# Performance work log

Measured on AMD Instinct MI355X. Metric: run time of the kernel, lower is better.

Reference implementation:

```python
import jax, jax.numpy as jnp
import numpy as np

DIM = 1024; DEPTH = 2; DSTATE = 128; HEADDIM = 64; DCONV = 4; EXPAND = 2
DINNER = EXPAND * DIM; NHEADS = DINNER // HEADDIM
CONVCH = DINNER + 2 * DSTATE          # x, B, C channels fed through depthwise conv
DINPROJ = 2 * DINNER + 2 * DSTATE + NHEADS  # z, xBC, dt
VOCAB = 256; EPS = 1e-5
B, T = 2, 1024


def _causal_conv(x, w, b):
    # depthwise causal conv1d: x [B,T,C], w [C,K], b [C]
    K = w.shape[1]
    xp = jnp.pad(x, ((0, 0), (K - 1, 0), (0, 0)))
    y = jnp.broadcast_to(b, x.shape)
    for k in range(K):
        y = y + xp[:, k:k + x.shape[1], :] * w[:, k]
    return y


def _mamba2_layer(h, Wp, cw, cb, dtb, alog, Dd, gw, Wo):
    Bb, Tt, _ = h.shape
    zxbcdt = jnp.einsum('btd,pd->btp', h, Wp)   # [B,T,DINPROJ]
    z = zxbcdt[..., :DINNER]
    xBC = zxbcdt[..., DINNER:DINNER + CONVCH]
    dt_raw = zxbcdt[..., DINNER + CONVCH:]
    xBC = jax.nn.silu(_causal_conv(xBC, cw, cb))
    xs = xBC[..., :DINNER].reshape(Bb, Tt, NHEADS, HEADDIM)
    Bm = xBC[..., DINNER:DINNER + DSTATE]        # [B,T,N] (ngroups=1)
    Cm = xBC[..., DINNER + DSTATE:]              # [B,T,N]
    dt = jax.nn.softplus(dt_raw + dtb)           # [B,T,H]
    dA = jnp.exp(dt * (-jnp.exp(alog)))          # [B,T,H]

    def step(s, inps):
        da_t, dt_t, x_t, b_t, c_t = inps
        dbx = dt_t[:, :, None, None] * x_t[..., None] * b_t[:, None, None, :]
        s = da_t[:, :, None, None] * s + dbx     # [B,H,P,N]
        y = jnp.einsum('bhpn,bn->bhp', s, c_t)
        return s, y

    s0 = jnp.zeros((Bb, NHEADS, HEADDIM, DSTATE), h.dtype)
    seq = (jnp.moveaxis(dA, 1, 0), jnp.moveaxis(dt, 1, 0), jnp.moveaxis(xs, 1, 0),
           jnp.moveaxis(Bm, 1, 0), jnp.moveaxis(Cm, 1, 0))
    _, ys = jax.lax.scan(step, s0, seq)          # ys [T,B,H,P]
    y = jnp.moveaxis(ys, 0, 1) + Dd[:, None] * xs
    y = y.reshape(Bb, Tt, DINNER) * jax.nn.silu(z)   # gated RMSNorm (norm(y*silu(z)))
    y = y * jax.lax.rsqrt(jnp.mean(y * y, -1, keepdims=True) + EPS) * gw
    return jnp.einsum('bti,di->btd', y, Wo)


def setup_inputs() -> dict:
    key = jax.random.key(0)
    ks = jax.random.split(key, 8)
    s = 0.02
    inp = {}
    inp['x'] = jax.random.randint(ks[0], (B, T), 0, VOCAB)
    inp['embed'] = jax.random.normal(ks[1], (VOCAB, DIM)) * s
    inp['in_proj_w'] = jax.random.normal(ks[2], (DEPTH, DINPROJ, DIM)) * s
    inp['conv_w'] = jax.random.normal(ks[3], (DEPTH, CONVCH, DCONV)) * 0.2
    inp['conv_b'] = jnp.zeros((DEPTH, CONVCH))
    # dt_bias so softplus(dt) ~ [1e-3, 1e-1]
    inp['dt_bias'] = jax.random.uniform(ks[4], (DEPTH, NHEADS), minval=-4.6, maxval=-2.0)
    inp['A_log'] = jnp.log(jnp.broadcast_to(jnp.arange(1, NHEADS + 1, dtype=jnp.float32), (DEPTH, NHEADS)))
    inp['D'] = jnp.ones((DEPTH, NHEADS))
    inp['gnorm_w'] = jnp.ones((DEPTH, DINNER))
    inp['out_proj_w'] = jax.random.normal(ks[5], (DEPTH, DIM, DINNER)) * s
    inp['final_norm_w'] = jnp.ones((DIM,))
    return inp


def reference(x, embed, in_proj_w, conv_w, conv_b, dt_bias, A_log, D, gnorm_w, out_proj_w, final_norm_w):
    h = embed[x]                                  # [B,T,DIM]
    for l in range(DEPTH):
        h = h + _mamba2_layer(h, in_proj_w[l], conv_w[l], conv_b[l], dt_bias[l],
                              A_log[l], D[l], gnorm_w[l], out_proj_w[l])
    h = h * jax.lax.rsqrt(jnp.mean(h * h, -1, keepdims=True) + EPS) * final_norm_w
    return jnp.einsum('btd,vd->btv', h, embed)    # tied head -> logits [B,T,256]
```

## Files before the change

kernel.cpp:

```cpp
#include <hip/hip_runtime.h>
#include <hip/hip_bf16.h>

#define BT 2048
#define T_SEQ 1024
#define DIM 1024
#define DINNER 2048
#define DSTATE 128
#define HEADDIM 64
#define NHEADS 32
#define CONVCH 2304
#define DINPROJ 4384
#define EPS_F 1e-5f
#define NCHUNK 16

typedef __bf16 bf16x8 __attribute__((ext_vector_type(8)));
typedef float f32x4 __attribute__((ext_vector_type(4)));

__device__ __forceinline__ float b2f(unsigned short u) {
  union { unsigned int i; float f; } v; v.i = ((unsigned int)u) << 16; return v.f;
}
__device__ __forceinline__ unsigned short f2b(float f) {
  unsigned int x = __float_as_uint(f);
  return (unsigned short)((x + 0x7fffu + ((x >> 16) & 1u)) >> 16);
}

__device__ __forceinline__ void gload_lds16(const void* g, void* l) {
  __builtin_amdgcn_global_load_lds(
      (const __attribute__((address_space(1))) unsigned int*)g,
      (__attribute__((address_space(3))) unsigned int*)l, 16, 0, 0);
}

#define NWP_ELEM (2 * DINPROJ * DIM)
#define NWO_ELEM (2 * DIM * DINNER)
#define NEM_ELEM (256 * DIM)
#define NWP_BLK (NWP_ELEM / 4 / 256)
#define NWO_BLK (NWO_ELEM / 4 / 256)
#define NEM_BLK (NEM_ELEM / 4 / 256)
#define PRO_BLK (NWP_BLK + NWO_BLK + NEM_BLK + BT)

__global__ void prologue_k(const float* __restrict__ Wp, const float* __restrict__ Wo,
                           const float* __restrict__ emb,
                           unsigned short* __restrict__ Wp_b,
                           unsigned short* __restrict__ Wo_b,
                           unsigned short* __restrict__ emb_b,
                           const int* __restrict__ x,
                           float* __restrict__ h, unsigned short* __restrict__ hb) {
  int bid = blockIdx.x;
  if (bid < NWP_BLK) {
    int i = (bid * 256 + threadIdx.x) * 4;
    float4 v = *(const float4*)(Wp + i);
    Wp_b[i + 0] = f2b(v.x); Wp_b[i + 1] = f2b(v.y);
    Wp_b[i + 2] = f2b(v.z); Wp_b[i + 3] = f2b(v.w);
  } else if (bid < NWP_BLK + NWO_BLK) {
    int i = ((bid - NWP_BLK) * 256 + threadIdx.x) * 4;
    float4 v = *(const float4*)(Wo + i);
    Wo_b[i + 0] = f2b(v.x); Wo_b[i + 1] = f2b(v.y);
    Wo_b[i + 2] = f2b(v.z); Wo_b[i + 3] = f2b(v.w);
  } else if (bid < NWP_BLK + NWO_BLK + NEM_BLK) {
    int i = ((bid - NWP_BLK - NWO_BLK) * 256 + threadIdx.x) * 4;
    float4 v = *(const float4*)(emb + i);
    emb_b[i + 0] = f2b(v.x); emb_b[i + 1] = f2b(v.y);
    emb_b[i + 2] = f2b(v.z); emb_b[i + 3] = f2b(v.w);
  } else {
    int t = bid - (NWP_BLK + NWO_BLK + NEM_BLK);
    int tok = x[t];
    int d = threadIdx.x;
#pragma unroll
    for (int j = 0; j < 4; ++j, d += 256) {
      float v = emb[(size_t)tok * DIM + d];
      h[(size_t)t * DIM + d] = v;
      hb[(size_t)t * DIM + d] = f2b(v);
    }
  }
}

template <int MODE, int TM, int TN>
__global__ __launch_bounds__(256) void gemm_bt(
    const unsigned short* __restrict__ A,
    const unsigned short* __restrict__ Bw,
    int M, int N, int K,
    unsigned short* __restrict__ Cout,
    float* __restrict__ aux,
    unsigned short* __restrict__ aux2) {
  constexpr int FM = TM / 32, FN = TN / 32;
  constexpr int JA = TM / 64, JB = TN / 64;
  constexpr int HA = TM * 32, HB = TN * 32;
  __shared__ __align__(16) unsigned short As[2 * HA];
  __shared__ __align__(16) unsigned short Bs[2 * HB];
  const int tid = threadIdx.x;
  const int lane = tid & 63;
  const int wave = tid >> 6;

  const int gx = gridDim.x, gy = gridDim.y;
  const int nwg = gx * gy;
  const int orig = (int)(blockIdx.y * gx + blockIdx.x);
  const int q = nwg >> 3, rr = nwg & 7;
  const int xcd = orig & 7, idx = orig >> 3;
  const int swz = (xcd < rr ? xcd * (q + 1) : rr * (q + 1) + (xcd - rr) * q) + idx;
  const int bxs = swz / gy;
  const int bys = swz - bxs * gy;
  const int m0 = bys * TM;
  const int n0 = bxs * TN;

  const int wm = (wave >> 1) * (TM / 2);
  const int wn = (wave & 1) * (TN / 2);
  const int quad = lane >> 4;
  const int r = lane & 15;

  f32x4 acc[FM][FN];
#pragma unroll
  for (int i = 0; i < FM; ++i)
#pragma unroll
    for (int j = 0; j < FN; ++j) acc[i][j] = f32x4{0.f, 0.f, 0.f, 0.f};

  const int rowt = tid >> 2, colt = (tid & 3) * 8;
  const unsigned short* aG[JA];
  unsigned short* aD[JA];
  const unsigned short* bG[JB];
  unsigned short* bD[JB];
#pragma unroll
  for (int j = 0; j < JA; ++j) {
    aG[j] = A + (size_t)(m0 + rowt + j * 64) * K + colt;
    aD[j] = As + wave * 512 + j * 2048;
  }
#pragma unroll
  for (int j = 0; j < JB; ++j) {
    int rb = n0 + rowt + j * 64; if (rb >= N) rb = N - 1;
    bG[j] = Bw + (size_t)rb * K + colt;
    bD[j] = Bs + wave * 512 + j * 2048;
  }

#pragma unroll
  for (int j = 0; j < JA; ++j) gload_lds16(aG[j], aD[j]);
#pragma unroll
  for (int j = 0; j < JB; ++j) gload_lds16(bG[j], bD[j]);
  __syncthreads();

  int cur = 0;
  for (int k0 = 0; k0 < K; k0 += 32) {
    const int nxt = cur ^ 1;
    if (k0 + 32 < K) {
#pragma unroll
      for (int j = 0; j < JA; ++j) gload_lds16(aG[j] + k0 + 32, aD[j] + nxt * HA);
#pragma unroll
      for (int j = 0; j < JB; ++j) gload_lds16(bG[j] + k0 + 32, bD[j] + nxt * HB);
    }
    const bf16x8* ap = (const bf16x8*)(As + cur * HA);
    const bf16x8* bp = (const bf16x8*)(Bs + cur * HB);
    bf16x8 af[FM], bfr[FN];
#pragma unroll
    for (int mt = 0; mt < FM; ++mt) af[mt] = ap[(wm + mt * 16 + r) * 4 + quad];
#pragma unroll
    for (int nt = 0; nt < FN; ++nt) bfr[nt] = bp[(wn + nt * 16 + r) * 4 + quad];
#pragma unroll
    for (int mt = 0; mt < FM; ++mt)
#pragma unroll
      for (int nt = 0; nt < FN; ++nt)
        acc[mt][nt] = __builtin_amdgcn_mfma_f32_16x16x32_bf16(af[mt], bfr[nt], acc[mt][nt], 0, 0, 0);
    __syncthreads();
    cur = nxt;
  }

#pragma unroll
  for (int mt = 0; mt < FM; ++mt) {
#pragma unroll
    for (int nt = 0; nt < FN; ++nt) {
#pragma unroll
      for (int i = 0; i < 4; ++i) {
        int gm = m0 + wm + mt * 16 + quad * 4 + i;
        int gn = n0 + wn + nt * 16 + r;
        if (gn < N) {
          float v = acc[mt][nt][i];
          if (MODE == 0) {
            Cout[(size_t)gm * N + gn] = f2b(v);
            if (gn >= DINNER + CONVCH)
              aux[(size_t)gm * NHEADS + (gn - (DINNER + CONVCH))] = v;
          } else if (MODE == 1) {
            size_t o = (size_t)gm * N + gn;
            float hnv = aux[o] + v;
            aux[o] = hnv;
            aux2[o] = f2b(hnv);
          } else {
            aux[(size_t)gm * N + gn] = v;
          }
        }
      }
    }
  }
}

__global__ void conv_k(const unsigned short* __restrict__ zx,
                       const float* __restrict__ cw,
                       const float* __restrict__ cb,
                       unsigned short* __restrict__ xbc,
                       unsigned short* __restrict__ bcb,
                       const float* __restrict__ dtraw,
                       const float* __restrict__ dtb,
                       const float* __restrict__ alog,
                       float* __restrict__ dtf,
                       float* __restrict__ lnAf) {
  int t = blockIdx.x;
  int tt = t & (T_SEQ - 1);
  if (threadIdx.x < NHEADS) {
    int h = threadIdx.x;
    float xx = dtraw[t * NHEADS + h] + dtb[h];
    float sp = (xx > 20.f) ? xx : log1pf(expf(xx));
    dtf[t * NHEADS + h] = sp;
    lnAf[t * NHEADS + h] = -sp * expf(alog[h]);
  }
  for (int c = threadIdx.x; c < CONVCH; c += 256) {
    float acc = cb[c];
#pragma unroll
    for (int k = 0; k < 4; ++k) {
      int tp = tt - 3 + k;
      if (tp >= 0)
        acc += b2f(zx[(size_t)(t - 3 + k) * DINPROJ + DINNER + c]) * cw[c * 4 + k];
    }
    float s = acc / (1.f + expf(-acc));
    unsigned short sb = f2b(s);
    xbc[(size_t)t * CONVCH + c] = sb;
    if (c >= DINNER) bcb[(size_t)t * 256 + (c - DINNER)] = sb;
  }
}

__global__ __launch_bounds__(256) void ssd_intra(
    const unsigned short* __restrict__ bcb,
    const unsigned short* __restrict__ xbc,
    const float* __restrict__ dtf, const float* __restrict__ lnAf,
    unsigned short* __restrict__ y1buf, unsigned short* __restrict__ SL,
    float* __restrict__ dtot) {
  const int bi = blockIdx.x;
  const int c = bi & 15;
  const int h = (bi >> 4) & 31;
  const int b = bi >> 9;
  const int tid = threadIdx.x;
  const int w = tid >> 6, l = tid & 63, r = l & 15, quad = l >> 4;
  const size_t tok0 = (size_t)b * T_SEQ + c * 64;

  __shared__ __align__(16) unsigned short BCs[64 * 264];
  __shared__ __align__(16) unsigned short Xrow[64 * 72];
  __shared__ __align__(16) unsigned short XTs[64 * 72];
  __shared__ __align__(16) unsigned short BWT[128 * 72];
  __shared__ __align__(16) unsigned short Ms[64 * 72];
  __shared__ float cumL[64], dtL[64], wsL[64];

#pragma unroll
  for (int i = 0; i < 8; ++i) {
    int idx = tid + i * 256;
    int row = idx >> 5, col = (idx & 31) * 8;
    uint4 v = *(const uint4*)(bcb + (tok0 + row) * 256 + col);
    *(uint4*)(BCs + row * 264 + col) = v;
  }
#pragma unroll
  for (int i = 0; i < 2; ++i) {
    int idx = tid + i * 256;
    int u = idx >> 3, pc = (idx & 7) * 8;
    uint4 v = *(const uint4*)(xbc + (tok0 + u) * CONVCH + h * HEADDIM + pc);
    *(uint4*)(Xrow + u * 72 + pc) = v;
  }
  if (tid < 64) {
    float dt = dtf[(tok0 + tid) * NHEADS + h];
    float v = lnAf[(tok0 + tid) * NHEADS + h];
    dtL[tid] = dt;
#pragma unroll
    for (int off = 1; off < 64; off <<= 1) {
      float u = __shfl_up(v, off, 64);
      if (tid >= off) v += u;
    }
    cumL[tid] = v;
    float tot = __shfl(v, 63, 64);
    wsL[tid] = dt * expf(tot - v);
    if (tid == 63) dtot[bi] = expf(tot);
  }
  __syncthreads();

#pragma unroll
  for (int i = 0; i < 2; ++i) {
    int idx = tid + i * 256;
    int p = idx >> 3, ug = (idx & 7) * 8;
    unsigned short tA[8];
#pragma unroll
    for (int j = 0; j < 8; ++j) tA[j] = Xrow[(ug + j) * 72 + p];
    *(uint4*)(XTs + p * 72 + ug) = *(uint4*)tA;
  }

  {
    const int n = tid >> 1;
    const int ug = (tid & 1) * 32;
    unsigned short eb[32];
#pragma unroll
    for (int j = 0; j < 32; ++j)
      eb[j] = f2b(b2f(BCs[(ug + j) * 264 + n]) * wsL[ug + j]);
#pragma unroll
    for (int qq = 0; qq < 4; ++qq)
      *(uint4*)(BWT + n * 72 + ug + qq * 8) = *(uint4*)(eb + qq * 8);
  }

  f32x4 g[4];
#pragma unroll
  for (int nt = 0; nt < 4; ++nt) g[nt] = f32x4{0.f, 0.f, 0.f, 0.f};
#pragma unroll
  for (int kk = 0; kk < 4; ++kk) {
    bf16x8 afr = *(const bf16x8*)(BCs + (w * 16 + r) * 264 + 128 + kk * 32 + quad * 8);
#pragma unroll
    for (int nt = 0; nt < 4; ++nt) {
      bf16x8 bfr = *(const bf16x8*)(BCs + (nt * 16 + r) * 264 + kk * 32 + quad * 8);
      g[nt] = __builtin_amdgcn_mfma_f32_16x16x32_bf16(afr, bfr, g[nt], 0, 0, 0);
    }
  }
#pragma unroll
  for (int nt = 0; nt < 4; ++nt) {
#pragma unroll
    for (int i = 0; i < 4; ++i) {
      int t_ = w * 16 + quad * 4 + i;
      int u_ = nt * 16 + r;
      float wv = (u_ <= t_) ? expf(cumL[t_] - cumL[u_]) * dtL[u_] : 0.f;
      Ms[t_ * 72 + u_] = f2b(g[nt][i] * wv);
    }
  }
  __syncthreads();

  f32x4 y1[4];
#pragma unroll
  for (int nt = 0; nt < 4; ++nt) y1[nt] = f32x4{0.f, 0.f, 0.f, 0.f};
#pragma unroll
  for (int kk = 0; kk < 2; ++kk) {
    bf16x8 afr = *(const bf16x8*)(Ms + (w * 16 + r) * 72 + kk * 32 + quad * 8);
#pragma unroll
    for (int nt = 0; nt < 4; ++nt) {
      bf16x8 bfr = *(const bf16x8*)(XTs + (nt * 16 + r) * 72 + kk * 32 + quad * 8);
      y1[nt] = __builtin_amdgcn_mfma_f32_16x16x32_bf16(afr, bfr, y1[nt], 0, 0, 0);
    }
  }
#pragma unroll
  for (int nt = 0; nt < 4; ++nt)
#pragma unroll
    for (int i = 0; i < 4; ++i) {
      int t_ = w * 16 + quad * 4 + i, p_ = nt * 16 + r;
      y1buf[((size_t)bi * 64 + t_) * 64 + p_] = f2b(y1[nt][i]);
    }

  f32x4 sl[8];
#pragma unroll
  for (int nt = 0; nt < 8; ++nt) sl[nt] = f32x4{0.f, 0.f, 0.f, 0.f};
#pragma unroll
  for (int kk = 0; kk < 2; ++kk) {
    bf16x8 afr = *(const bf16x8*)(XTs + (w * 16 + r) * 72 + kk * 32 + quad * 8);
#pragma unroll
    for (int nt = 0; nt < 8; ++nt) {
      bf16x8 bfr = *(const bf16x8*)(BWT + (nt * 16 + r) * 72 + kk * 32 + quad * 8);
      sl[nt] = __builtin_amdgcn_mfma_f32_16x16x32_bf16(afr, bfr, sl[nt], 0, 0, 0);
    }
  }
#pragma unroll
  for (int nt = 0; nt < 8; ++nt)
#pragma unroll
    for (int i = 0; i < 4; ++i) {
      int p_ = w * 16 + quad * 4 + i, n_ = nt * 16 + r;
      SL[((size_t)bi * 64 + p_) * 128 + n_] = f2b(sl[nt][i]);
    }
}

__global__ void ssd_state(unsigned short* __restrict__ SL,
                          const float* __restrict__ dtot) {
  int gidx = blockIdx.x * 256 + threadIdx.x;
  int n4 = (gidx & 31) * 4;
  int p = (gidx >> 5) & 63;
  int bh = gidx >> 11;
  float sx = 0.f, sy = 0.f, sz = 0.f, sw = 0.f;
  for (int c = 0; c < NCHUNK; ++c) {
    size_t off = ((size_t)(bh * 16 + c) * 64 + p) * 128 + n4;
    uint2 lv = *(uint2*)(SL + off);
    float d = dtot[bh * 16 + c];
    uint2 sv;
    sv.x = (unsigned)f2b(sx) | ((unsigned)f2b(sy) << 16);
    sv.y = (unsigned)f2b(sz) | ((unsigned)f2b(sw) << 16);
    *(uint2*)(SL + off) = sv;
    sx = d * sx + b2f(lv.x & 0xffff);
    sy = d * sy + b2f(lv.x >> 16);
    sz = d * sz + b2f(lv.y & 0xffff);
    sw = d * sw + b2f(lv.y >> 16);
  }
}

__global__ __launch_bounds__(256) void ssd_inter(
    const unsigned short* __restrict__ bcb,
    const unsigned short* __restrict__ SL,
    const unsigned short* __restrict__ y1buf,
    const unsigned short* __restrict__ xbc,
    const unsigned short* __restrict__ zx,
    const float* __restrict__ lnAf,
    const float* __restrict__ Dw,
    unsigned short* __restrict__ yg) {
  const int bi = blockIdx.x;
  const int c = bi & 15, h = (bi >> 4) & 31, b = bi >> 9;
  const int tid = threadIdx.x;
  const int w = tid >> 6, l = tid & 63, r = l & 15, quad = l >> 4;
  const size_t tok0 = (size_t)b * T_SEQ + c * 64;

  __shared__ __align__(16) unsigned short Cs[64 * 136];
  __shared__ __align__(16) unsigned short Sp[64 * 136];
  __shared__ __align__(16) float Yf[64 * 68];
  __shared__ float cumL[64];

#pragma unroll
  for (int i = 0; i < 4; ++i) {
    int idx = tid + i * 256;
    int row = idx >> 4, col = (idx & 15) * 8;
    uint4 v = *(const uint4*)(bcb + (tok0 + row) * 256 + 128 + col);
    *(uint4*)(Cs + row * 136 + col) = v;
    uint4 s = *(const uint4*)(SL + ((size_t)bi * 64 + row) * 128 + col);
    *(uint4*)(Sp + row * 136 + col) = s;
  }
  if (tid < 64) {
    float v = lnAf[(tok0 + tid) * NHEADS + h];
#pragma unroll
    for (int off = 1; off < 64; off <<= 1) {
      float u = __shfl_up(v, off, 64);
      if (tid >= off) v += u;
    }
    cumL[tid] = v;
  }
  __syncthreads();

  f32x4 yi[4];
#pragma unroll
  for (int nt = 0; nt < 4; ++nt) yi[nt] = f32x4{0.f, 0.f, 0.f, 0.f};
#pragma unroll
  for (int kk = 0; kk < 4; ++kk) {
    bf16x8 afr = *(const bf16x8*)(Cs + (w * 16 + r) * 136 + kk * 32 + quad * 8);
#pragma unroll
    for (int nt = 0; nt < 4; ++nt) {
      bf16x8 bfr = *(const bf16x8*)(Sp + (nt * 16 + r) * 136 + kk * 32 + quad * 8);
      yi[nt] = __builtin_amdgcn_mfma_f32_16x16x32_bf16(afr, bfr, yi[nt], 0, 0, 0);
    }
  }
#pragma unroll
  for (int nt = 0; nt < 4; ++nt)
#pragma unroll
    for (int i = 0; i < 4; ++i) {
      int t_ = w * 16 + quad * 4 + i, p_ = nt * 16 + r;
      float y1 = b2f(y1buf[((size_t)bi * 64 + t_) * 64 + p_]);
      Yf[t_ * 68 + p_] = y1 + expf(cumL[t_]) * yi[nt][i];
    }
  __syncthreads();

  const float Dh = Dw[h];
  const int t_ = tid >> 2, pg = (tid & 3) * 16;
  const size_t tok = tok0 + t_;
  union { uint4 q[2]; unsigned short u[16]; } xv, zv, ov;
  xv.q[0] = *(const uint4*)(xbc + tok * CONVCH + h * 64 + pg);
  xv.q[1] = *(const uint4*)(xbc + tok * CONVCH + h * 64 + pg + 8);
  zv.q[0] = *(const uint4*)(zx + tok * DINPROJ + h * 64 + pg);
  zv.q[1] = *(const uint4*)(zx + tok * DINPROJ + h * 64 + pg + 8);
#pragma unroll
  for (int j = 0; j < 16; ++j) {
    float y = Yf[t_ * 68 + pg + j] + Dh * b2f(xv.u[j]);
    float zf = b2f(zv.u[j]);
    ov.u[j] = f2b(y * (zf / (1.f + expf(-zf))));
  }
  *(uint4*)(yg + tok * DINNER + h * 64 + pg) = ov.q[0];
  *(uint4*)(yg + tok * DINNER + h * 64 + pg + 8) = ov.q[1];
}

__global__ void rms2048_k(const unsigned short* __restrict__ in,
                          const float* __restrict__ w,
                          unsigned short* __restrict__ out) {
  int t = blockIdx.x;
  int base = threadIdx.x * 8;
  union { uint4 q; unsigned short u[8]; } vv;
  vv.q = *(const uint4*)(in + (size_t)t * DINNER + base);
  float f[8];
  float ss = 0.f;
#pragma unroll
  for (int j = 0; j < 8; ++j) { f[j] = b2f(vv.u[j]); ss += f[j] * f[j]; }
#pragma unroll
  for (int o = 32; o > 0; o >>= 1) ss += __shfl_xor(ss, o, 64);
  __shared__ float red[4];
  if ((threadIdx.x & 63) == 0) red[threadIdx.x >> 6] = ss;
  __syncthreads();
  ss = red[0] + red[1] + red[2] + red[3];
  float scale = rsqrtf(ss * (1.f / DINNER) + EPS_F);
#pragma unroll
  for (int j = 0; j < 8; ++j)
    out[(size_t)t * DINNER + base + j] = f2b(f[j] * scale * w[base + j]);
}

__global__ void rmsfinal_k(const float* __restrict__ hf,
                           const float* __restrict__ w,
                           unsigned short* __restrict__ out) {
  int t = blockIdx.x;
  int base = threadIdx.x * 4;
  float4 v = *(const float4*)(hf + (size_t)t * DIM + base);
  float ss = v.x * v.x + v.y * v.y + v.z * v.z + v.w * v.w;
#pragma unroll
  for (int o = 32; o > 0; o >>= 1) ss += __shfl_xor(ss, o, 64);
  __shared__ float red[4];
  if ((threadIdx.x & 63) == 0) red[threadIdx.x >> 6] = ss;
  __syncthreads();
  ss = red[0] + red[1] + red[2] + red[3];
  float scale = rsqrtf(ss * (1.f / DIM) + EPS_F);
  out[(size_t)t * DIM + base + 0] = f2b(v.x * scale * w[base + 0]);
  out[(size_t)t * DIM + base + 1] = f2b(v.y * scale * w[base + 1]);
  out[(size_t)t * DIM + base + 2] = f2b(v.z * scale * w[base + 2]);
  out[(size_t)t * DIM + base + 3] = f2b(v.w * scale * w[base + 3]);
}

extern "C" void kernel_launch(void* const* d_in, const int* in_sizes, int n_in,
                              void* d_out, int out_size, void* d_ws, size_t ws_size,
                              hipStream_t stream) {
  const int*   x    = (const int*)d_in[0];
  const float* emb  = (const float*)d_in[1];
  const float* Wp   = (const float*)d_in[2];
  const float* cw   = (const float*)d_in[3];
  const float* cb   = (const float*)d_in[4];
  const float* dtb  = (const float*)d_in[5];
  const float* alog = (const float*)d_in[6];
  const float* Dw   = (const float*)d_in[7];
  const float* gw   = (const float*)d_in[8];
  const float* Wo   = (const float*)d_in[9];
  const float* fnw  = (const float*)d_in[10];

  char* w = (char*)d_ws;
  auto alloc = [&](size_t bytes) {
    char* p = w; w += (bytes + 255) & ~(size_t)255; return p;
  };
  float* h_f32          = (float*)alloc((size_t)BT * DIM * 4);
  unsigned short* hb    = (unsigned short*)alloc((size_t)BT * DIM * 2);
  unsigned short* zx    = (unsigned short*)alloc((size_t)BT * DINPROJ * 2);
  float* dtraw          = (float*)alloc((size_t)BT * NHEADS * 4);
  float* dtf            = (float*)alloc((size_t)BT * NHEADS * 4);
  float* lnAf           = (float*)alloc((size_t)BT * NHEADS * 4);
  unsigned short* xbc   = (unsigned short*)alloc((size_t)BT * CONVCH * 2);
  unsigned short* bcb   = (unsigned short*)alloc((size_t)BT * 256 * 2);
  unsigned short* SL    = (unsigned short*)alloc((size_t)1024 * 64 * 128 * 2);
  unsigned short* y1buf = (unsigned short*)alloc((size_t)1024 * 64 * 64 * 2);
  float* dtot           = (float*)alloc((size_t)1024 * 4);
  unsigned short* yg    = (unsigned short*)alloc((size_t)BT * DINNER * 2);
  unsigned short* yn    = (unsigned short*)alloc((size_t)BT * DINNER * 2);
  unsigned short* hn    = (unsigned short*)alloc((size_t)BT * DIM * 2);
  unsigned short* Wp_b  = (unsigned short*)alloc((size_t)2 * DINPROJ * DIM * 2);
  unsigned short* Wo_b  = (unsigned short*)alloc((size_t)2 * DIM * DINNER * 2);
  unsigned short* emb_b = (unsigned short*)alloc((size_t)256 * DIM * 2 + 256);

  prologue_k<<<PRO_BLK, 256, 0, stream>>>(Wp, Wo, emb, Wp_b, Wo_b, emb_b, x, h_f32, hb);

  for (int l = 0; l < 2; ++l) {
    const unsigned short* Wpl = Wp_b + (size_t)l * DINPROJ * DIM;
    const unsigned short* Wol = Wo_b + (size_t)l * DIM * DINNER;
    const float* cwl   = cw + (size_t)l * CONVCH * 4;
    const float* cbl   = cb + (size_t)l * CONVCH;
    const float* dtbl  = dtb + l * NHEADS;
    const float* alogl = alog + l * NHEADS;
    const float* Dwl   = Dw + l * NHEADS;
    const float* gwl   = gw + (size_t)l * DINNER;

    gemm_bt<0, 128, 128><<<dim3(35, 16), 256, 0, stream>>>(hb, Wpl, BT, DINPROJ, DIM, zx, dtraw, nullptr);
    conv_k<<<BT, 256, 0, stream>>>(zx, cwl, cbl, xbc, bcb, dtraw, dtbl, alogl, dtf, lnAf);
    ssd_intra<<<1024, 256, 0, stream>>>(bcb, xbc, dtf, lnAf, y1buf, SL, dtot);
    ssd_state<<<512, 256, 0, stream>>>(SL, dtot);
    ssd_inter<<<1024, 256, 0, stream>>>(bcb, SL, y1buf, xbc, zx, lnAf, Dwl, yg);
    rms2048_k<<<BT, 256, 0, stream>>>(yg, gwl, yn);
    gemm_bt<1, 64, 64><<<dim3(16, 32), 256, 0, stream>>>(yn, Wol, BT, DIM, DINNER, nullptr, h_f32, hb);
  }

  rmsfinal_k<<<BT, 256, 0, stream>>>(h_f32, fnw, hn);
  gemm_bt<2, 64, 64><<<dim3(4, 32), 256, 0, stream>>>(hn, emb_b, BT, 256, DIM,
                                                      nullptr, (float*)d_out, nullptr);
}
```

Baseline: 371.4 us.

## Fuse gated RMSNorm into out-projection via per-token sum-of-squares and prescaled weights

```diff
diff --git a/kernel.cpp b/kernel.cpp
--- a/kernel.cpp
+++ b/kernel.cpp
@@ -39,7 +39,7 @@
 #define PRO_BLK (NWP_BLK + NWO_BLK + NEM_BLK + BT)
 
 __global__ void prologue_k(const float* __restrict__ Wp, const float* __restrict__ Wo,
-                           const float* __restrict__ emb,
+                           const float* __restrict__ emb, const float* __restrict__ gw,
                            unsigned short* __restrict__ Wp_b,
                            unsigned short* __restrict__ Wo_b,
                            unsigned short* __restrict__ emb_b,
@@ -53,9 +53,12 @@
     Wp_b[i + 2] = f2b(v.z); Wp_b[i + 3] = f2b(v.w);
   } else if (bid < NWP_BLK + NWO_BLK) {
     int i = ((bid - NWP_BLK) * 256 + threadIdx.x) * 4;
+    int li = i / (DIM * DINNER);
+    int kk = i & (DINNER - 1);
     float4 v = *(const float4*)(Wo + i);
-    Wo_b[i + 0] = f2b(v.x); Wo_b[i + 1] = f2b(v.y);
-    Wo_b[i + 2] = f2b(v.z); Wo_b[i + 3] = f2b(v.w);
+    float4 g = *(const float4*)(gw + li * DINNER + kk);
+    Wo_b[i + 0] = f2b(v.x * g.x); Wo_b[i + 1] = f2b(v.y * g.y);
+    Wo_b[i + 2] = f2b(v.z * g.z); Wo_b[i + 3] = f2b(v.w * g.w);
   } else if (bid < NWP_BLK + NWO_BLK + NEM_BLK) {
     int i = ((bid - NWP_BLK - NWO_BLK) * 256 + threadIdx.x) * 4;
     float4 v = *(const float4*)(emb + i);
@@ -81,7 +84,8 @@
     int M, int N, int K,
     unsigned short* __restrict__ Cout,
     float* __restrict__ aux,
-    unsigned short* __restrict__ aux2) {
+    unsigned short* __restrict__ aux2,
+    const float* __restrict__ ssq) {
   constexpr int FM = TM / 32, FN = TN / 32;
   constexpr int JA = TM / 64, JB = TN / 64;
   constexpr int HA = TM * 32, HB = TN * 32;
@@ -176,8 +180,9 @@
             if (gn >= DINNER + CONVCH)
               aux[(size_t)gm * NHEADS + (gn - (DINNER + CONVCH))] = v;
           } else if (MODE == 1) {
+            float scl = rsqrtf(ssq[gm] * (1.f / DINNER) + EPS_F);
             size_t o = (size_t)gm * N + gn;
-            float hnv = aux[o] + v;
+            float hnv = aux[o] + v * scl;
             aux[o] = hnv;
             aux2[o] = f2b(hnv);
           } else {
@@ -198,9 +203,11 @@
                        const float* __restrict__ dtb,
                        const float* __restrict__ alog,
                        float* __restrict__ dtf,
-                       float* __restrict__ lnAf) {
+                       float* __restrict__ lnAf,
+                       float* __restrict__ ssq) {
   int t = blockIdx.x;
   int tt = t & (T_SEQ - 1);
+  if (threadIdx.x == 0) ssq[t] = 0.f;
   if (threadIdx.x < NHEADS) {
     int h = threadIdx.x;
     float xx = dtraw[t * NHEADS + h] + dtb[h];
@@ -391,7 +398,8 @@
     const unsigned short* __restrict__ zx,
     const float* __restrict__ lnAf,
     const float* __restrict__ Dw,
-    unsigned short* __restrict__ yg) {
+    unsigned short* __restrict__ yg,
+    float* __restrict__ ssq) {
   const int bi = blockIdx.x;
   const int c = bi & 15, h = (bi >> 4) & 31, b = bi >> 9;
   const int tid = threadIdx.x;
@@ -453,37 +461,20 @@
   xv.q[1] = *(const uint4*)(xbc + tok * CONVCH + h * 64 + pg + 8);
   zv.q[0] = *(const uint4*)(zx + tok * DINPROJ + h * 64 + pg);
   zv.q[1] = *(const uint4*)(zx + tok * DINPROJ + h * 64 + pg + 8);
+  float ssf = 0.f;
 #pragma unroll
   for (int j = 0; j < 16; ++j) {
     float y = Yf[t_ * 68 + pg + j] + Dh * b2f(xv.u[j]);
     float zf = b2f(zv.u[j]);
-    ov.u[j] = f2b(y * (zf / (1.f + expf(-zf))));
+    float yg_f = y * (zf / (1.f + expf(-zf)));
+    ov.u[j] = f2b(yg_f);
+    ssf += yg_f * yg_f;
   }
   *(uint4*)(yg + tok * DINNER + h * 64 + pg) = ov.q[0];
   *(uint4*)(yg + tok * DINNER + h * 64 + pg + 8) = ov.q[1];
-}
-
-__global__ void rms2048_k(const unsigned short* __restrict__ in,
-                          const float* __restrict__ w,
-                          unsigned short* __restrict__ out) {
-  int t = blockIdx.x;
-  int base = threadIdx.x * 8;
-  union { uint4 q; unsigned short u[8]; } vv;
-  vv.q = *(const uint4*)(in + (size_t)t * DINNER + base);
-  float f[8];
-  float ss = 0.f;
-#pragma unroll
-  for (int j = 0; j < 8; ++j) { f[j] = b2f(vv.u[j]); ss += f[j] * f[j]; }
-#pragma unroll
-  for (int o = 32; o > 0; o >>= 1) ss += __shfl_xor(ss, o, 64);
-  __shared__ float red[4];
-  if ((threadIdx.x & 63) == 0) red[threadIdx.x >> 6] = ss;
-  __syncthreads();
-  ss = red[0] + red[1] + red[2] + red[3];
-  float scale = rsqrtf(ss * (1.f / DINNER) + EPS_F);
-#pragma unroll
-  for (int j = 0; j < 8; ++j)
-    out[(size_t)t * DINNER + base + j] = f2b(f[j] * scale * w[base + j]);
+  ssf += __shfl_xor(ssf, 1, 64);
+  ssf += __shfl_xor(ssf, 2, 64);
+  if ((tid & 3) == 0) atomicAdd(&ssq[tok], ssf);
 }
 
 __global__ void rmsfinal_k(const float* __restrict__ hf,
@@ -537,13 +528,13 @@
   unsigned short* y1buf = (unsigned short*)alloc((size_t)1024 * 64 * 64 * 2);
   float* dtot           = (float*)alloc((size_t)1024 * 4);
   unsigned short* yg    = (unsigned short*)alloc((size_t)BT * DINNER * 2);
-  unsigned short* yn    = (unsigned short*)alloc((size_t)BT * DINNER * 2);
+  float* ssq            = (float*)alloc((size_t)BT * 4);
   unsigned short* hn    = (unsigned short*)alloc((size_t)BT * DIM * 2);
   unsigned short* Wp_b  = (unsigned short*)alloc((size_t)2 * DINPROJ * DIM * 2);
   unsigned short* Wo_b  = (unsigned short*)alloc((size_t)2 * DIM * DINNER * 2);
   unsigned short* emb_b = (unsigned short*)alloc((size_t)256 * DIM * 2 + 256);
 
-  prologue_k<<<PRO_BLK, 256, 0, stream>>>(Wp, Wo, emb, Wp_b, Wo_b, emb_b, x, h_f32, hb);
+  prologue_k<<<PRO_BLK, 256, 0, stream>>>(Wp, Wo, emb, gw, Wp_b, Wo_b, emb_b, x, h_f32, hb);
 
   for (int l = 0; l < 2; ++l) {
     const unsigned short* Wpl = Wp_b + (size_t)l * DINPROJ * DIM;
@@ -553,18 +544,16 @@
     const float* dtbl  = dtb + l * NHEADS;
     const float* alogl = alog + l * NHEADS;
     const float* Dwl   = Dw + l * NHEADS;
-    const float* gwl   = gw + (size_t)l * DINNER;
-
-    gemm_bt<0, 128, 128><<<dim3(35, 16), 256, 0, stream>>>(hb, Wpl, BT, DINPROJ, DIM, zx, dtraw, nullptr);
-    conv_k<<<BT, 256, 0, stream>>>(zx, cwl, cbl, xbc, bcb, dtraw, dtbl, alogl, dtf, lnAf);
+
+    gemm_bt<0, 128, 128><<<dim3(35, 16), 256, 0, stream>>>(hb, Wpl, BT, DINPROJ, DIM, zx, dtraw, nullptr, nullptr);
+    conv_k<<<BT, 256, 0, stream>>>(zx, cwl, cbl, xbc, bcb, dtraw, dtbl, alogl, dtf, lnAf, ssq);
     ssd_intra<<<1024, 256, 0, stream>>>(bcb, xbc, dtf, lnAf, y1buf, SL, dtot);
     ssd_state<<<512, 256, 0, stream>>>(SL, dtot);
-    ssd_inter<<<1024, 256, 0, stream>>>(bcb, SL, y1buf, xbc, zx, lnAf, Dwl, yg);
-    rms2048_k<<<BT, 256, 0, stream>>>(yg, gwl, yn);
-    gemm_bt<1, 64, 64><<<dim3(16, 32), 256, 0, stream>>>(yn, Wol, BT, DIM, DINNER, nullptr, h_f32, hb);
+    ssd_inter<<<1024, 256, 0, stream>>>(bcb, SL, y1buf, xbc, zx, lnAf, Dwl, yg, ssq);
+    gemm_bt<1, 64, 64><<<dim3(16, 32), 256, 0, stream>>>(yg, Wol, BT, DIM, DINNER, nullptr, h_f32, hb, ssq);
   }
 
   rmsfinal_k<<<BT, 256, 0, stream>>>(h_f32, fnw, hn);
   gemm_bt<2, 64, 64><<<dim3(4, 32), 256, 0, stream>>>(hn, emb_b, BT, 256, DIM,
-                                                      nullptr, (float*)d_out, nullptr);
-}
+                                                      nullptr, (float*)d_out, nullptr, nullptr);
+}
```

New measurement: 364.6 us (median of 2 runs). About the same (-1.8%).
